# Kernel tuning notes

Hardware: AMD Instinct MI355X
Metric: run time of the kernel (lower is better)

## Reference

```python
import jax, jax.numpy as jnp
import numpy as np
from jax import lax

# norse LIFParameters defaults: dt=1e-3, tau_mem_inv=100, tau_syn_inv=200, v_leak=0, v_reset=0
ALPHA = 100.0
DT_TM = 0.1   # dt * tau_mem_inv
DT_TS = 0.2   # dt * tau_syn_inv

@jax.custom_vjp
def superspike(x):
    # Heaviside forward, SuperSpike surrogate gradient backward
    return (x > 0).astype(x.dtype)

def _ss_fwd(x):
    return superspike(x), x

def _ss_bwd(x, g):
    return (g / (ALPHA * jnp.abs(x) + 1.0) ** 2,)

superspike.defvjp(_ss_fwd, _ss_bwd)

def lif_step(inp, v, i, v_th):
    # norse lif_feed_forward_step (feedforward LIF cell)
    v_dec = v + DT_TM * (i - v)           # v_leak = 0
    i_dec = i * (1.0 - DT_TS)
    z = superspike(v_dec - v_th)
    v_new = (1.0 - z) * v_dec             # reset to v_reset = 0 on spike
    return z, v_new, i_dec + inp

def conv2d(x, w):
    return lax.conv_general_dilated(x, w, (1, 1), 'VALID',
                                    dimension_numbers=('NCHW', 'OIHW', 'NCHW'))

def avg_pool2(x):
    s = lax.reduce_window(x, jnp.zeros((), x.dtype), lax.add,
                          (1, 1, 2, 2), (1, 1, 2, 2), 'VALID')
    return s * jnp.asarray(0.25, x.dtype)

def setup_inputs() -> dict:
    key = jax.random.key(0)
    ks = jax.random.split(key, 6)
    x = jax.random.uniform(ks[0], (40, 256, 1, 28, 28), dtype=jnp.float32)
    # kaiming-ish scales (1/sqrt(fan_in))
    w_conv1 = jax.random.normal(ks[1], (20, 1, 3, 3), jnp.float32) * (1.0 / np.sqrt(9))
    w_conv2 = jax.random.normal(ks[2], (50, 20, 3, 3), jnp.float32) * (1.0 / np.sqrt(180))
    w_fc1 = jax.random.normal(ks[3], (500, 6050), jnp.float32) * (1.0 / np.sqrt(6050))
    w_fc2 = jax.random.normal(ks[4], (200, 500), jnp.float32) * (1.0 / np.sqrt(500))
    w_fc_out = jax.random.normal(ks[5], (10, 200), jnp.float32) * (1.0 / np.sqrt(200))
    return {"x": x, "w_conv1": w_conv1, "w_conv2": w_conv2,
            "w_fc1": w_fc1, "w_fc2": w_fc2, "w_fc_out": w_fc_out}

def reference(x, w_conv1, w_conv2, w_fc1, w_fc2, w_fc_out):
    T, B = x.shape[0], x.shape[1]
    dt = x.dtype
    z0 = jnp.zeros((B, 20, 26, 26), dt)
    z1 = jnp.zeros((B, 50, 11, 11), dt)
    z2 = jnp.zeros((B, 500), dt)
    z3 = jnp.zeros((B, 200), dt)
    zo = jnp.zeros((B, 10), dt)
    carry0 = (z0, z0, z1, z1, z2, z2, z3, z3, zo, zo)

    def step(carry, xt):
        v0, i0, v1, i1, v2, i2, v3, i3, vo, io = carry
        z = conv2d(xt, w_conv1)
        z, v0, i0 = lif_step(z, v0, i0, 0.2)
        z = avg_pool2(z)
        z = conv2d(z, w_conv2)
        z, v1, i1 = lif_step(z, v1, i1, 0.2)
        z = z.reshape(B, -1)                      # [B, 50*11*11]
        z = z @ w_fc1.T
        z, v2, i2 = lif_step(z, v2, i2, 0.1)
        z = z @ w_fc2.T
        z, v3, i3 = lif_step(z, v3, i3, 0.05)
        z = z @ w_fc_out.T
        # LICell (norse li_feed_forward_step): output is decayed membrane voltage
        v_dec = vo + DT_TM * (io - vo)
        i_new = io * (1.0 - DT_TS) + z
        return (v0, i0, v1, i1, v2, i2, v3, i3, v_dec, i_new), v_dec

    _, voltages = lax.scan(step, carry0, x)
    return voltages  # [T, B, output_neurons]
```

## Files before the change

### kernel.cpp

```cpp
#include <hip/hip_runtime.h>
#include <hip/hip_bf16.h>

typedef _Float16 f16x8 __attribute__((ext_vector_type(8)));
typedef float f32x4  __attribute__((ext_vector_type(4)));
typedef unsigned short u16x4 __attribute__((ext_vector_type(4)));

#define T_STEPS 40
#define BATCH   256
#define S2LO    0.000244140625f

__device__ __forceinline__ unsigned short f2h_bits(float f) {
    union { _Float16 h; unsigned short u; } c; c.h = (_Float16)f; return c.u;
}

__device__ __forceinline__ float lif_update(float inp, float& v, float& i, float vth) {
    float vd = __fadd_rn(v, __fmul_rn(0.1f, __fsub_rn(i, v)));
    float id = __fmul_rn(0.8f, i);
    float z  = (vd > vth) ? 1.0f : 0.0f;
    v = (vd > vth) ? 0.0f : vd;
    i = __fadd_rn(id, inp);
    return z;
}

__device__ __forceinline__ void llds16(const unsigned short* g, void* l) {
    __builtin_amdgcn_global_load_lds(
        (const __attribute__((address_space(1))) unsigned int*)g,
        (__attribute__((address_space(3))) unsigned int*)l, 16, 0, 0);
}

__global__ __launch_bounds__(512) void k_conv1(
    const float* __restrict__ x,
    const float* __restrict__ w1,
    unsigned char* __restrict__ s0)
{
    const int b    = blockIdx.y;
    const int tid  = threadIdx.x;
    const int cell = blockIdx.x*512 + tid;
    const bool active = cell < 3380;
    const int pos  = cell / 20;
    const int oc   = cell % 20;
    const int pr   = pos / 13, q = pos % 13;
    const int r0   = 2*pr, c0 = 2*q;

    __shared__ __align__(16) float xl[2][784];

    float wr[9];
    if (active) {
        #pragma unroll
        for (int j = 0; j < 9; ++j) wr[j] = w1[oc*9 + j];
    }
    float vs[2][2], is[2][2];
    #pragma unroll
    for (int dr = 0; dr < 2; ++dr)
        #pragma unroll
        for (int dc = 0; dc < 2; ++dc) { vs[dr][dc] = 0.f; is[dr][dc] = 0.f; }

    if (tid < 196) {
        const float4* xs4 = (const float4*)(x + (size_t)b*784);
        *(float4*)&xl[0][tid*4] = xs4[tid];
    }

    for (int t = 0; t < T_STEPS; ++t) {
        __syncthreads();
        if (t + 1 < T_STEPS && tid < 196) {
            const float4* xs4 = (const float4*)(x + (size_t)((t+1)*BATCH + b)*784);
            *(float4*)&xl[(t+1)&1][tid*4] = xs4[tid];
        }
        const float* xc = xl[t&1];
        size_t base = (size_t)(t*BATCH + b) * 4096;

        if (active) {
            float tle[4][4];
            #pragma unroll
            for (int r = 0; r < 4; ++r)
                #pragma unroll
                for (int c = 0; c < 4; ++c)
                    tle[r][c] = xc[(r0 + r)*28 + c0 + c];
            int zsum = 0;
            #pragma unroll
            for (int dr = 0; dr < 2; ++dr)
                #pragma unroll
                for (int dc = 0; dc < 2; ++dc) {
                    float acc = 0.f;
                    #pragma unroll
                    for (int kr = 0; kr < 3; ++kr)
                        #pragma unroll
                        for (int kc = 0; kc < 3; ++kc)
                            acc += tle[dr+kr][dc+kc] * wr[kr*3+kc];
                    float z = lif_update(acc, vs[dr][dc], is[dr][dc], 0.2f);
                    zsum += (z > 0.5f) ? 1 : 0;
                }
            s0[base + (size_t)pos*24 + oc] = (unsigned char)zsum;
        } else {
            int p2 = cell - 3380;
            for (int idx = p2; idx < 716; idx += 204) {
                if (idx < 676) s0[base + (size_t)(idx >> 2)*24 + 20 + (idx & 3)] = 0;
                else           s0[base + 4056 + (idx - 676)] = 0;
            }
        }
    }
}

__global__ __launch_bounds__(256, 2) void k_conv2(
    const unsigned char* __restrict__ s0,
    const float* __restrict__ w2,
    unsigned short* __restrict__ z1)
{
    const int b    = blockIdx.x >> 1;
    const int half = blockIdx.x & 1;
    const int tid  = threadIdx.x;
    const int wv   = tid >> 6;
    const int lane = tid & 63;
    const int l15  = lane & 15;
    const int kg   = lane >> 4;
    const int wm   = wv;

    __shared__ __align__(16) unsigned short w2h[32*232];
    __shared__ __align__(16) unsigned short w2m[32*232];
    __shared__ __align__(16) unsigned short sIn[2*4096];

    for (int s = tid; s < 32*232; s += 256) {
        int ocw = s / 232, kk = s % 232;
        int g = kk / 24, ic = kk % 24;
        int oc = half*32 + ocw;
        float val = 0.f;
        if (oc < 50 && g < 9 && ic < 20) val = w2[(oc*20 + ic)*9 + g];
        _Float16 h = (_Float16)val;
        float r1 = (val - (float)h) * 4096.0f;
        union { _Float16 h; unsigned short u; } ch, cm;
        ch.h = h; cm.h = (_Float16)r1;
        w2h[s] = ch.u;
        w2m[s] = cm.u;
    }

    f16x8 bfrH[2][7];
    int addrA[2][7];
    #pragma unroll
    for (int mt = 0; mt < 2; ++mt) {
        int pos = wm*32 + mt*16 + l15;
        #pragma unroll
        for (int kt = 0; kt < 7; ++kt) {
            int k = kt*32 + kg*8;
            int g = k / 24, o = k - g*24;
            if (pos <= 120 && g <= 8) {
                int in_idx = pos + 2*(pos/11) + 13*(g/3) + (g % 3);
                addrA[mt][kt] = in_idx*48 + o*2;
            } else addrA[mt][kt] = 8128;
        }
    }

    {
        const unsigned char* srow = s0 + (size_t)(0*BATCH + b)*4096;
        uint4 raw = *(const uint4*)(srow + tid*16);
        unsigned short hv[16];
        #pragma unroll
        for (int w = 0; w < 4; ++w) {
            unsigned int u = ((const unsigned int*)&raw)[w];
            #pragma unroll
            for (int j = 0; j < 4; ++j)
                hv[w*4+j] = f2h_bits(0.25f * (float)((u >> (8*j)) & 0xFFu));
        }
        unsigned short* dst = sIn + tid*16;
        *(f16x8*)dst       = *(const f16x8*)&hv[0];
        *(f16x8*)(dst + 8) = *(const f16x8*)&hv[8];
    }
    __syncthreads();

    #pragma unroll
    for (int nt = 0; nt < 2; ++nt) {
        int n = nt*16 + l15;
        #pragma unroll
        for (int kt = 0; kt < 7; ++kt)
            bfrH[nt][kt] = *(const f16x8*)&w2h[n*232 + kt*32 + kg*8];
    }

    float vst[2][2][4], ist[2][2][4];
    #pragma unroll
    for (int mt = 0; mt < 2; ++mt)
        #pragma unroll
        for (int nt = 0; nt < 2; ++nt)
            #pragma unroll
            for (int r = 0; r < 4; ++r) { vst[mt][nt][r] = 0.f; ist[mt][nt][r] = 0.f; }

    const f32x4 zero4 = {0.f, 0.f, 0.f, 0.f};

    for (int t = 0; t < T_STEPS; ++t) {
        if (t > 0) __syncthreads();

        uint4 raw;
        if (t + 1 < T_STEPS)
            raw = *(const uint4*)(s0 + (size_t)((t+1)*BATCH + b)*4096 + tid*16);

        const char* curB = (const char*)(sIn + (t&1)*4096);

        f32x4 acch[2][2], accl[2][2];
        #pragma unroll
        for (int mt = 0; mt < 2; ++mt)
            #pragma unroll
            for (int nt = 0; nt < 2; ++nt) { acch[mt][nt] = zero4; accl[mt][nt] = zero4; }

        #pragma unroll
        for (int kt = 0; kt < 7; ++kt) {
            f16x8 bm[2];
            #pragma unroll
            for (int nt = 0; nt < 2; ++nt) {
                int n = nt*16 + l15, k = kt*32 + kg*8;
                bm[nt] = *(const f16x8*)&w2m[n*232 + k];
            }
            #pragma unroll
            for (int mt = 0; mt < 2; ++mt) {
                f16x8 a = *(const f16x8*)(curB + addrA[mt][kt]);
                #pragma unroll
                for (int nt = 0; nt < 2; ++nt) {
                    acch[mt][nt] = __builtin_amdgcn_mfma_f32_16x16x32_f16(
                        a, bfrH[nt][kt], acch[mt][nt], 0, 0, 0);
                    accl[mt][nt] = __builtin_amdgcn_mfma_f32_16x16x32_f16(
                        a, bm[nt], accl[mt][nt], 0, 0, 0);
                }
            }
        }

        size_t rowoff = (size_t)(t*BATCH + b) * 6208;
        #pragma unroll
        for (int mt = 0; mt < 2; ++mt) {
            int posb = wm*32 + mt*16 + kg*4;
            #pragma unroll
            for (int nt = 0; nt < 2; ++nt) {
                int ocn = half*32 + nt*16 + l15;
                u16x4 pack;
                #pragma unroll
                for (int r = 0; r < 4; ++r) {
                    float inp = __fadd_rn(acch[mt][nt][r], __fmul_rn(S2LO, accl[mt][nt][r]));
                    float z = lif_update(inp, vst[mt][nt][r], ist[mt][nt][r], 0.2f);
                    int pos = posb + r;
                    pack[r] = (pos <= 120 && z > 0.5f) ? (unsigned short)0x3C00 : (unsigned short)0;
                }
                if (ocn < 50 && posb < 121)
                    *(u16x4*)(z1 + rowoff + ocn*124 + posb) = pack;
            }
        }
        if (half == 0 && tid < 8) z1[rowoff + 6200 + tid] = 0;

        if (t + 1 < T_STEPS) {
            unsigned short hv[16];
            #pragma unroll
            for (int w = 0; w < 4; ++w) {
                unsigned int u = ((const unsigned int*)&raw)[w];
                #pragma unroll
                for (int j = 0; j < 4; ++j)
                    hv[w*4+j] = f2h_bits(0.25f * (float)((u >> (8*j)) & 0xFFu));
            }
            unsigned short* dst = sIn + ((t+1)&1)*4096 + tid*16;
            *(f16x8*)dst       = *(const f16x8*)&hv[0];
            *(f16x8*)(dst + 8) = *(const f16x8*)&hv[8];
        }
    }
}

__global__ __launch_bounds__(256, 3) void k_gemm(
    const unsigned short* __restrict__ A,
    const unsigned short* __restrict__ B0,
    float* __restrict__ C0,
    int Kp, int kiters, int ldc, int nstore,
    size_t strideB, size_t strideC)
{
    __shared__ __align__(16) unsigned short As[128*64];
    __shared__ __align__(16) unsigned short Bs[128*64];
    const unsigned short* B = B0 + (size_t)blockIdx.z * strideB;
    float* C = C0 + (size_t)blockIdx.z * strideC;

    const int tid  = threadIdx.x;
    const int lane = tid & 63;
    const int wv   = tid >> 6;
    const int wm   = wv & 1, wn = wv >> 1;
    const int l15  = lane & 15, kg = lane >> 4;
    const int mbase = blockIdx.x * 128;
    const int nbase = blockIdx.y * 128;

    const f32x4 zero4 = {0.f, 0.f, 0.f, 0.f};
    f32x4 acc[4][4];
    #pragma unroll
    for (int mt = 0; mt < 4; ++mt)
        #pragma unroll
        for (int nt = 0; nt < 4; ++nt) acc[mt][nt] = zero4;

    const int rowA = tid >> 3;
    const int sw   = (((tid & 7) ^ (rowA & 7))) * 8;
    char* ldsA = (char*)As + (size_t)wv*1024;
    char* ldsB = (char*)Bs + (size_t)wv*1024;

    for (int ki = 0; ki < kiters; ++ki) {
        int kb = ki * 64;
        #pragma unroll
        for (int c = 0; c < 4; ++c) {
            int row = c*32 + rowA;
            llds16(A + (size_t)(mbase + row)*Kp + kb + sw, ldsA + c*4096);
            llds16(B + (size_t)(nbase + row)*Kp + kb + sw, ldsB + c*4096);
        }
        __syncthreads();
        #pragma unroll
        for (int kt = 0; kt < 2; ++kt) {
            f16x8 bfv[4], afv[4];
            #pragma unroll
            for (int nt = 0; nt < 4; ++nt) {
                int rb = wn*64 + nt*16 + l15;
                int ch = ((kt*4 + kg) ^ (rb & 7)) * 8;
                bfv[nt] = *(const f16x8*)&Bs[rb*64 + ch];
            }
            #pragma unroll
            for (int mt = 0; mt < 4; ++mt) {
                int ra = wm*64 + mt*16 + l15;
                int ch = ((kt*4 + kg) ^ (ra & 7)) * 8;
                afv[mt] = *(const f16x8*)&As[ra*64 + ch];
            }
            #pragma unroll
            for (int mt = 0; mt < 4; ++mt)
                #pragma unroll
                for (int nt = 0; nt < 4; ++nt)
                    acc[mt][nt] = __builtin_amdgcn_mfma_f32_16x16x32_f16(
                        afv[mt], bfv[nt], acc[mt][nt], 0, 0, 0);
        }
        __syncthreads();
    }

    #pragma unroll
    for (int mt = 0; mt < 4; ++mt) {
        int m0 = mbase + wm*64 + mt*16 + kg*4;
        #pragma unroll
        for (int nt = 0; nt < 4; ++nt) {
            int n = nbase + wn*64 + nt*16 + l15;
            if (n < nstore) {
                #pragma unroll
                for (int r = 0; r < 4; ++r)
                    C[(size_t)(m0 + r)*ldc + n] = acc[mt][nt][r];
            }
        }
    }
}

__global__ void k_pack(const float* __restrict__ src,
                       unsigned short* __restrict__ hi, unsigned short* __restrict__ lo,
                       int N, int K, int Kp, int total) {
    int idx = blockIdx.x*256 + threadIdx.x;
    if (idx >= total) return;
    int n = idx / Kp, k = idx - n*Kp;
    float v = (n < N && k < K) ? src[n*K + k] : 0.f;
    _Float16 h = (_Float16)v;
    float r1 = (v - (float)h) * 4096.0f;
    union { _Float16 h; unsigned short u; } ch, cl;
    ch.h = h; cl.h = (_Float16)r1;
    hi[idx] = ch.u;
    lo[idx] = cl.u;
}

__global__ void k_pack_fc1(const float* __restrict__ src,
                           unsigned short* __restrict__ hi, unsigned short* __restrict__ lo,
                           int total) {
    int idx = blockIdx.x*256 + threadIdx.x;
    if (idx >= total) return;
    int n = idx / 6208, k = idx - n*6208;
    int oc = k / 124, pos = k - oc*124;
    float v = (n < 500 && oc < 50 && pos < 121) ? src[n*6050 + oc*121 + pos] : 0.f;
    _Float16 h = (_Float16)v;
    float r1 = (v - (float)h) * 4096.0f;
    union { _Float16 h; unsigned short u; } ch, cl;
    ch.h = h; cl.h = (_Float16)r1;
    hi[idx] = ch.u;
    lo[idx] = cl.u;
}

__global__ __launch_bounds__(512) void k_lif_scan(
    const float* __restrict__ c0, size_t pstride,
    unsigned short* __restrict__ zout,
    int ld, int nvalid, float vth)
{
    int b = blockIdx.x;
    int n = threadIdx.x;
    float v = 0.f, cur = 0.f;
    for (int t = 0; t < T_STEPS; ++t) {
        size_t idx = (size_t)(t*BATCH + b)*ld + n;
        float s = __fadd_rn(c0[idx], __fmul_rn(S2LO, c0[idx + pstride]));
        float z = lif_update(s, v, cur, vth);
        zout[idx] = (n < nvalid && z > 0.5f) ? (unsigned short)0x3C00 : (unsigned short)0;
    }
}

__global__ void k_li(const float* __restrict__ c0, size_t pstride, float* __restrict__ out) {
    int g = blockIdx.x*64 + threadIdx.x;
    if (g >= 2560) return;
    int b = g / 10, n = g - b*10;
    float vo = 0.f, io = 0.f;
    for (int t = 0; t < T_STEPS; ++t) {
        size_t idx = (size_t)(t*BATCH + b)*16 + n;
        float s = __fadd_rn(c0[idx], __fmul_rn(S2LO, c0[idx + pstride]));
        float vd = __fadd_rn(vo, __fmul_rn(0.1f, __fsub_rn(io, vo)));
        out[(size_t)(t*BATCH + b)*10 + n] = vd;
        io = __fadd_rn(__fmul_rn(0.8f, io), s);
        vo = vd;
    }
}

extern "C" void kernel_launch(void* const* d_in, const int* in_sizes, int n_in,
                              void* d_out, int out_size, void* d_ws, size_t ws_size,
                              hipStream_t stream) {
    (void)in_sizes; (void)n_in; (void)out_size; (void)ws_size;
    const float* x   = (const float*)d_in[0];
    const float* w1  = (const float*)d_in[1];
    const float* w2  = (const float*)d_in[2];
    const float* wf1 = (const float*)d_in[3];
    const float* wf2 = (const float*)d_in[4];
    const float* wfo = (const float*)d_in[5];
    char* ws = (char*)d_ws;

    unsigned short* z1    = (unsigned short*)(ws);
    unsigned char*  s0    = (unsigned char*)(ws + 127139840);
    unsigned short* W1hi  = (unsigned short*)(ws + 127139840);
    unsigned short* W2hi  = (unsigned short*)(ws + 139853824);
    unsigned short* Wohi  = (unsigned short*)(ws + 140378112);
    float*          c2p   = (float*)(ws + 140509184);
    unsigned short* z2    = (unsigned short*)(ws);
    float*          c3p   = (float*)(ws + 10485760);
    unsigned short* z3    = (unsigned short*)(ws + 31457280);
    float*          c4p   = (float*)(ws + 36700160);

    k_conv1<<<dim3(7, 256), 512, 0, stream>>>(x, w1, s0);
    k_conv2<<<512, 256, 0, stream>>>(s0, w2, z1);

    k_pack_fc1<<<(3178496+255)/256, 256, 0, stream>>>(wf1, W1hi, W1hi+3178496, 3178496);
    k_pack<<<(131072+255)/256, 256, 0, stream>>>(wf2, W2hi, W2hi+131072, 200, 500, 512, 131072);
    k_pack<<<(32768+255)/256,  256, 0, stream>>>(wfo, Wohi, Wohi+32768,  10,  200, 256, 32768);

    k_gemm<<<dim3(80,4,2), 256, 0, stream>>>(z1, W1hi, c2p, 6208, 97, 512, 512,
                                             (size_t)3178496, (size_t)5242880);
    k_lif_scan<<<256, 512, 0, stream>>>(c2p, (size_t)5242880, z2, 512, 500, 0.1f);
    k_gemm<<<dim3(80,2,2), 256, 0, stream>>>(z2, W2hi, c3p, 512, 8, 256, 256,
                                             (size_t)131072, (size_t)2621440);
    k_lif_scan<<<256, 256, 0, stream>>>(c3p, (size_t)2621440, z3, 256, 200, 0.05f);
    k_gemm<<<dim3(80,1,2), 256, 0, stream>>>(z3, Wohi, c4p, 256, 4, 16, 16,
                                             (size_t)32768, (size_t)163840);
    k_li<<<40, 64, 0, stream>>>(c4p, (size_t)163840, (float*)d_out);
}
```

Baseline: 404.3 us.

## Fuse hi/lo fc1 weight GEMMs sharing A tiles and split K across z

Adds a dedicated fc1 GEMM that loads each activation tile once and multiplies it against both the high and low fp16 weight planes, combining them in the epilogue. The z grid dimension now splits K into two halves instead of selecting the weight plane, and the LIF scan sums the partials with unit scale. This removes the duplicate reads of the large spike matrix and changes the tile shape to 128x64. The cost is more accumulator registers per thread and a different occupancy target.

```diff
diff --git a/kernel.cpp b/kernel.cpp
--- a/kernel.cpp
+++ b/kernel.cpp
@@ -257,6 +257,97 @@
     }
 }
 
+__global__ __launch_bounds__(256, 4) void k_gemm_fc1(
+    const unsigned short* __restrict__ A,
+    const unsigned short* __restrict__ Bhi,
+    const unsigned short* __restrict__ Blo,
+    float* __restrict__ P)
+{
+    __shared__ __align__(16) unsigned short As[128*64];
+    __shared__ __align__(16) unsigned short Bh[64*64];
+    __shared__ __align__(16) unsigned short Bl[64*64];
+
+    const int tid  = threadIdx.x;
+    const int lane = tid & 63;
+    const int wv   = tid >> 6;
+    const int wm   = wv & 1, wn = wv >> 1;
+    const int l15  = lane & 15, kg = lane >> 4;
+    const int mbase = blockIdx.x * 128;
+    const int nbase = blockIdx.y * 64;
+    const int kz    = blockIdx.z;
+    const int kb0   = kz * 3136;
+    const int kiters = 49 - kz;
+
+    float* Pz = P + (size_t)kz * 5242880;
+
+    const f32x4 zero4 = {0.f, 0.f, 0.f, 0.f};
+    f32x4 acch[4][2], accl[4][2];
+    #pragma unroll
+    for (int mt = 0; mt < 4; ++mt)
+        #pragma unroll
+        for (int nt = 0; nt < 2; ++nt) { acch[mt][nt] = zero4; accl[mt][nt] = zero4; }
+
+    const int rowA = tid >> 3;
+    const int sw   = (((tid & 7) ^ (rowA & 7))) * 8;
+    char* ldsA = (char*)As + (size_t)wv*1024;
+    char* ldsH = (char*)Bh + (size_t)wv*1024;
+    char* ldsL = (char*)Bl + (size_t)wv*1024;
+
+    for (int ki = 0; ki < kiters; ++ki) {
+        int kb = kb0 + ki * 64;
+        #pragma unroll
+        for (int c = 0; c < 4; ++c)
+            llds16(A + (size_t)(mbase + c*32 + rowA)*6208 + kb + sw, ldsA + c*4096);
+        #pragma unroll
+        for (int c = 0; c < 2; ++c) {
+            llds16(Bhi + (size_t)(nbase + c*32 + rowA)*6208 + kb + sw, ldsH + c*4096);
+            llds16(Blo + (size_t)(nbase + c*32 + rowA)*6208 + kb + sw, ldsL + c*4096);
+        }
+        __syncthreads();
+        #pragma unroll
+        for (int kt = 0; kt < 2; ++kt) {
+            f16x8 bh[2], bl[2], afv[4];
+            #pragma unroll
+            for (int nt = 0; nt < 2; ++nt) {
+                int rb = wn*32 + nt*16 + l15;
+                int ch = ((kt*4 + kg) ^ (rb & 7)) * 8;
+                bh[nt] = *(const f16x8*)&Bh[rb*64 + ch];
+                bl[nt] = *(const f16x8*)&Bl[rb*64 + ch];
+            }
+            #pragma unroll
+            for (int mt = 0; mt < 4; ++mt) {
+                int ra = wm*64 + mt*16 + l15;
+                int ch = ((kt*4 + kg) ^ (ra & 7)) * 8;
+                afv[mt] = *(const f16x8*)&As[ra*64 + ch];
+            }
+            #pragma unroll
+            for (int mt = 0; mt < 4; ++mt)
+                #pragma unroll
+                for (int nt = 0; nt < 2; ++nt) {
+                    acch[mt][nt] = __builtin_amdgcn_mfma_f32_16x16x32_f16(
+                        afv[mt], bh[nt], acch[mt][nt], 0, 0, 0);
+                    accl[mt][nt] = __builtin_amdgcn_mfma_f32_16x16x32_f16(
+                        afv[mt], bl[nt], accl[mt][nt], 0, 0, 0);
+                }
+        }
+        __syncthreads();
+    }
+
+    #pragma unroll
+    for (int mt = 0; mt < 4; ++mt) {
+        int m0 = mbase + wm*64 + mt*16 + kg*4;
+        #pragma unroll
+        for (int nt = 0; nt < 2; ++nt) {
+            int n = nbase + wn*32 + nt*16 + l15;
+            #pragma unroll
+            for (int r = 0; r < 4; ++r) {
+                float s = __fadd_rn(acch[mt][nt][r], __fmul_rn(S2LO, accl[mt][nt][r]));
+                Pz[(size_t)(m0 + r)*512 + n] = s;
+            }
+        }
+    }
+}
+
 __global__ __launch_bounds__(256, 3) void k_gemm(
     const unsigned short* __restrict__ A,
     const unsigned short* __restrict__ B0,
@@ -372,14 +463,14 @@
 __global__ __launch_bounds__(512) void k_lif_scan(
     const float* __restrict__ c0, size_t pstride,
     unsigned short* __restrict__ zout,
-    int ld, int nvalid, float vth)
+    int ld, int nvalid, float vth, float pscale)
 {
     int b = blockIdx.x;
     int n = threadIdx.x;
     float v = 0.f, cur = 0.f;
     for (int t = 0; t < T_STEPS; ++t) {
         size_t idx = (size_t)(t*BATCH + b)*ld + n;
-        float s = __fadd_rn(c0[idx], __fmul_rn(S2LO, c0[idx + pstride]));
+        float s = __fadd_rn(c0[idx], __fmul_rn(pscale, c0[idx + pstride]));
         float z = lif_update(s, v, cur, vth);
         zout[idx] = (n < nvalid && z > 0.5f) ? (unsigned short)0x3C00 : (unsigned short)0;
     }
@@ -430,12 +521,11 @@
     k_pack<<<(131072+255)/256, 256, 0, stream>>>(wf2, W2hi, W2hi+131072, 200, 500, 512, 131072);
     k_pack<<<(32768+255)/256,  256, 0, stream>>>(wfo, Wohi, Wohi+32768,  10,  200, 256, 32768);
 
-    k_gemm<<<dim3(80,4,2), 256, 0, stream>>>(z1, W1hi, c2p, 6208, 97, 512, 512,
-                                             (size_t)3178496, (size_t)5242880);
-    k_lif_scan<<<256, 512, 0, stream>>>(c2p, (size_t)5242880, z2, 512, 500, 0.1f);
+    k_gemm_fc1<<<dim3(80, 8, 2), 256, 0, stream>>>(z1, W1hi, W1hi+3178496, c2p);
+    k_lif_scan<<<256, 512, 0, stream>>>(c2p, (size_t)5242880, z2, 512, 500, 0.1f, 1.0f);
     k_gemm<<<dim3(80,2,2), 256, 0, stream>>>(z2, W2hi, c3p, 512, 8, 256, 256,
                                              (size_t)131072, (size_t)2621440);
-    k_lif_scan<<<256, 256, 0, stream>>>(c3p, (size_t)2621440, z3, 256, 200, 0.05f);
+    k_lif_scan<<<256, 256, 0, stream>>>(c3p, (size_t)2621440, z3, 256, 200, 0.05f, S2LO);
     k_gemm<<<dim3(80,1,2), 256, 0, stream>>>(z3, Wohi, c4p, 256, 4, 16, 16,
                                              (size_t)32768, (size_t)163840);
     k_li<<<40, 64, 0, stream>>>(c4p, (size_t)163840, (float*)d_out);
```

Measured after the change: 408.4 us. No clear change (+1.0%).
